# Performance work log

Measured on AMD Instinct MI355X. Metric: run time of the kernel, lower is better.

## Reference

```python
import jax, jax.numpy as jnp
import numpy as np

TOP_K = 2  # config.num_active_experts


def setup_inputs() -> dict:
    key = jax.random.key(0)
    k1, k2, k3, k4 = jax.random.split(key, 4)
    B, S, D = 2, 2048, 1024
    E, W = 8, 1024  # 8 experts, each width 1024 -> total_expert_width = 8192
    x = jax.random.normal(k1, (B, S, D), dtype=jnp.float32)
    router_w = jax.random.normal(k2, (E, D), dtype=jnp.float32) * 0.02
    w1 = jax.random.normal(k3, (D, E * W), dtype=jnp.float32) * 0.02
    w2 = jax.random.normal(k4, (E * W, D), dtype=jnp.float32) * 0.02
    return {"x": x, "router_w": router_w, "w1": w1, "w2": w2}


def reference(x, router_w, w1, w2):
    B, S, D = x.shape
    E = router_w.shape[0]
    W = w1.shape[1] // E  # uniform expert width
    T = B * S
    xf = x.reshape(T, D)

    # Router: sigmoid gating, top-k, sum-normalized weights (norm_topk_prob)
    router_logits = jnp.einsum('td,ed->te', xf, router_w)
    router_probs = jax.nn.sigmoid(router_logits.astype(jnp.float32))
    top_w, sel = jax.lax.top_k(router_probs, TOP_K)          # [T,K]
    top_w = top_w / (top_w.sum(axis=-1, keepdims=True) + 1e-20)
    top_w = top_w.astype(x.dtype)

    # Expert MLPs: expert e uses w1[:, off_e:off_e+W], w2[off_e:off_e+W, :].
    # Uniform width -> single batched einsum over experts (same math as the
    # padded-gather / block-sparse SDD/DSD grouped GEMM pipeline).
    W1e = w1.reshape(D, E, W).transpose(1, 0, 2)             # [E,D,W]
    W2e = w2.reshape(E, W, D)                                # [E,W,D]
    h = jnp.einsum('td,edw->etw', xf, W1e)                   # up-proj
    a = jnp.square(jax.nn.relu(h))                           # relu_squared
    y = jnp.einsum('etw,ewd->etd', a, W2e)                   # down-proj

    # Weighted scatter-combine: combine_weights[t,e] = top_w if e selected else 0
    cw = jnp.zeros((T, E), dtype=x.dtype).at[jnp.arange(T)[:, None], sel].set(top_w)
    out = jnp.einsum('etd,te->td', y, cw)
    return out.reshape(B, S, D)
```

## Files before the change

### kernel.cpp

```cpp
#include <hip/hip_runtime.h>
#include <hip/hip_bf16.h>


#define T_TOKENS 4096
#define DD 1024
#define EE 8
#define WW 1024
#define CAP 1536
#define BM 128
#define BN 64
#define BK 64
#define MT (CAP / BM)
#define NT 16

typedef short bf16x8 __attribute__((ext_vector_type(8)));
typedef float f32x4 __attribute__((ext_vector_type(4)));

__device__ __forceinline__ void gload_lds16(const void* g, void* l) {
  __builtin_amdgcn_global_load_lds((__attribute__((address_space(1))) void*)(g),
                                   (__attribute__((address_space(3))) void*)(l),
                                   16, 0, 0);
}

__device__ __forceinline__ float bf2f(unsigned short u) {
  union { unsigned int i; float f; } v; v.i = (unsigned int)u << 16; return v.f;
}

#define TR_BLOCKS 4096
__global__ __launch_bounds__(256) void pre_kernel(
    const float* __restrict__ w1, const float* __restrict__ w2,
    const float* __restrict__ x, const float* __restrict__ rw,
    __hip_bfloat16* __restrict__ w1t, __hip_bfloat16* __restrict__ w2t,
    __hip_bfloat16* __restrict__ xb, int* __restrict__ sel,
    float* __restrict__ wpair)
{
  __shared__ float tile[64][65];
  int b = blockIdx.x;
  if (b < TR_BLOCKS) {
    int bx = b & 15;
    int by = b >> 4;
    const float* src; __hip_bfloat16* dst;
    long src_ld, dst_ld, c0, r0;
    if (by < 128) {
      src = w1; dst = w1t; src_ld = EE * WW; dst_ld = DD;
      c0 = (long)bx * 64;
      r0 = (long)by * 64;
    } else {
      int z = by - 128;
      int e = z >> 4;
      int yy = z & 15;
      src = w2 + (long)e * WW * DD;
      dst = w2t + (long)e * DD * WW;
      src_ld = DD; dst_ld = WW;
      c0 = (long)bx * 64;
      r0 = (long)yy * 64;
    }
    int tx = threadIdx.x & 15, ty = threadIdx.x >> 4;
#pragma unroll
    for (int i = 0; i < 4; i++) {
      int sr = ty + 16 * i;
      f32x4 v = *(const f32x4*)(src + (c0 + sr) * src_ld + r0 + tx * 4);
      tile[sr][tx * 4 + 0] = v[0];
      tile[sr][tx * 4 + 1] = v[1];
      tile[sr][tx * 4 + 2] = v[2];
      tile[sr][tx * 4 + 3] = v[3];
    }
    __syncthreads();
#pragma unroll
    for (int i = 0; i < 4; i++) {
      int dr = ty + 16 * i;
      union { __hip_bfloat16 hb[4]; ushort4 u4; } pk;
#pragma unroll
      for (int j = 0; j < 4; j++)
        pk.hb[j] = __float2bfloat16(tile[tx * 4 + j][dr]);
      *(ushort4*)((unsigned short*)dst + (r0 + dr) * dst_ld + c0 + tx * 4) = pk.u4;
    }
  } else {
    int lane = threadIdx.x & 63;
    int wave = threadIdx.x >> 6;
    int t = (b - TR_BLOCKS) * 4 + wave;
    const float* xrow = x + (size_t)t * DD;
    float acc[EE];
#pragma unroll
    for (int e = 0; e < EE; e++) acc[e] = 0.f;
#pragma unroll
    for (int i = 0; i < DD / 64; i++) {
      int d = lane + i * 64;
      float xv = xrow[d];
      xb[t * DD + d] = __float2bfloat16(xv);
#pragma unroll
      for (int e = 0; e < EE; e++) acc[e] += xv * rw[e * DD + d];
    }
#pragma unroll
    for (int e = 0; e < EE; e++) {
#pragma unroll
      for (int off = 32; off > 0; off >>= 1)
        acc[e] += __shfl_down(acc[e], off, 64);
    }
    if (lane == 0) {
      float p[EE];
#pragma unroll
      for (int e = 0; e < EE; e++) p[e] = 1.f / (1.f + expf(-acc[e]));
      int e0 = 0; float b0 = p[0];
      for (int e = 1; e < EE; e++) if (p[e] > b0) { b0 = p[e]; e0 = e; }
      int e1 = -1; float b1 = -1.f;
      for (int e = 0; e < EE; e++) {
        if (e == e0) continue;
        if (p[e] > b1) { b1 = p[e]; e1 = e; }
      }
      float s = b0 + b1 + 1e-20f;
      sel[t] = e0 | (e1 << 8);
      wpair[2 * t]     = b0 / s;
      wpair[2 * t + 1] = b1 / s;
    }
  }
}

__global__ __launch_bounds__(1024) void build_lists(
    const int* __restrict__ sel, int* __restrict__ counts,
    int* __restrict__ idx, int* __restrict__ tslot)
{
  __shared__ int lcnt[EE];
  int tid = threadIdx.x, lane = tid & 63;
  if (tid < EE) lcnt[tid] = 0;
  __syncthreads();
  unsigned long long lower = (1ull << lane) - 1;
#pragma unroll
  for (int j = 0; j < T_TOKENS / 1024; j++) {
    int t = j * 1024 + tid;
    int s = sel[t];
    int e0 = s & 0xff, e1 = (s >> 8) & 0xff;
    int slot0 = 0, slot1 = 0;
#pragma unroll
    for (int e = 0; e < EE; e++) {
      unsigned long long m0 = __ballot(e0 == e);
      unsigned long long m1 = __ballot(e1 == e);
      int c0 = __popcll(m0), c1 = __popcll(m1);
      int base = 0;
      if (lane == 0 && (c0 + c1) > 0) base = atomicAdd(&lcnt[e], c0 + c1);
      base = __shfl(base, 0, 64);
      if (e0 == e) slot0 = base + __popcll(m0 & lower);
      if (e1 == e) slot1 = base + c0 + __popcll(m1 & lower);
    }
    int p0 = e0 * CAP + slot0, p1 = e1 * CAP + slot1;
    idx[p0] = t; idx[p1] = t;
    tslot[2 * t] = p0; tslot[2 * t + 1] = p1;
  }
  __syncthreads();
  if (tid < EE) counts[tid] = lcnt[tid];
}

__global__ __launch_bounds__(256) void gemm1_kernel(
    const __hip_bfloat16* __restrict__ xb, const __hip_bfloat16* __restrict__ w1t,
    const int* __restrict__ counts, const int* __restrict__ idx,
    __hip_bfloat16* __restrict__ act)
{
  __shared__ short As[BM * BK];
  __shared__ short Bs[BN * BK];
  int bid = blockIdx.x;
  int e = bid & 7;
  int i = bid >> 3;
  int mt = i >> 4, nt = i & 15;
  int n_e = counts[e];
  if (mt * BM >= n_e) return;

  int tid = threadIdx.x;
  int lane = tid & 63;
  int wave = __builtin_amdgcn_readfirstlane(tid >> 6);
  int wm = (wave >> 1) * 64, wn = (wave & 1) * 32;
  int m16 = lane & 15, qd = lane >> 4;

  const __hip_bfloat16* gA[4];
  const __hip_bfloat16* gB[2];
#pragma unroll
  for (int i2 = 0; i2 < 4; i2++) {
    int s = i2 * 256 + tid;
    int r = s >> 3;
    int q = (s & 7) ^ (r & 7);
    int rowA = mt * BM + r;
    int slot = rowA < n_e ? rowA : n_e - 1;
    int tok = idx[e * CAP + slot];
    gA[i2] = xb + (size_t)tok * DD + q * 8;
  }
#pragma unroll
  for (int i2 = 0; i2 < 2; i2++) {
    int s = i2 * 256 + tid;
    int r = s >> 3;
    int q = (s & 7) ^ (r & 7);
    gB[i2] = w1t + ((size_t)e * WW + nt * BN + r) * DD + q * 8;
  }
  short* ldsA[4];
  short* ldsB[2];
#pragma unroll
  for (int i2 = 0; i2 < 4; i2++) ldsA[i2] = As + (i2 * 256 + wave * 64) * 8;
#pragma unroll
  for (int i2 = 0; i2 < 2; i2++) ldsB[i2] = Bs + (i2 * 256 + wave * 64) * 8;

  int aoff[4][2], boff[2][2];
#pragma unroll
  for (int i2 = 0; i2 < 4; i2++) {
    int r = wm + i2 * 16 + m16;
#pragma unroll
    for (int h = 0; h < 2; h++)
      aoff[i2][h] = (r * 8 + ((qd + h * 4) ^ (r & 7))) * 8;
  }
#pragma unroll
  for (int j = 0; j < 2; j++) {
    int r = wn + j * 16 + m16;
#pragma unroll
    for (int h = 0; h < 2; h++)
      boff[j][h] = (r * 8 + ((qd + h * 4) ^ (r & 7))) * 8;
  }

  f32x4 zero = {0.f, 0.f, 0.f, 0.f};
  f32x4 acc[4][2];
#pragma unroll
  for (int mi = 0; mi < 4; mi++)
#pragma unroll
    for (int ni = 0; ni < 2; ni++) acc[mi][ni] = zero;

  for (int k0 = 0; k0 < DD; k0 += BK) {
    gload_lds16(gA[0] + k0, ldsA[0]);
    gload_lds16(gA[1] + k0, ldsA[1]);
    gload_lds16(gA[2] + k0, ldsA[2]);
    gload_lds16(gA[3] + k0, ldsA[3]);
    gload_lds16(gB[0] + k0, ldsB[0]);
    gload_lds16(gB[1] + k0, ldsB[1]);
    __syncthreads();
#pragma unroll
    for (int h = 0; h < 2; h++) {
      bf16x8 af[4], bfr[2];
#pragma unroll
      for (int i2 = 0; i2 < 4; i2++) af[i2] = *(const bf16x8*)(As + aoff[i2][h]);
#pragma unroll
      for (int j = 0; j < 2; j++) bfr[j] = *(const bf16x8*)(Bs + boff[j][h]);
#pragma unroll
      for (int mi = 0; mi < 4; mi++)
#pragma unroll
        for (int ni = 0; ni < 2; ni++)
          acc[mi][ni] = __builtin_amdgcn_mfma_f32_16x16x32_bf16(
              af[mi], bfr[ni], acc[mi][ni], 0, 0, 0);
    }
    __syncthreads();
  }

#pragma unroll
  for (int mi = 0; mi < 4; mi++) {
#pragma unroll
    for (int reg = 0; reg < 4; reg++) {
      int rowt = mt * BM + wm + mi * 16 + qd * 4 + reg;
      if (rowt < n_e) {
#pragma unroll
        for (int ni = 0; ni < 2; ni++) {
          float v = acc[mi][ni][reg];
          v = v > 0.f ? v * v : 0.f;
          int col = nt * BN + wn + ni * 16 + m16;
          act[((size_t)e * CAP + rowt) * WW + col] = __float2bfloat16(v);
        }
      }
    }
  }
}

__global__ __launch_bounds__(256) void gemm2_kernel(
    const __hip_bfloat16* __restrict__ act, const __hip_bfloat16* __restrict__ w2t,
    const int* __restrict__ counts, __hip_bfloat16* __restrict__ y)
{
  __shared__ short As[BM * BK];
  __shared__ short Bs[BN * BK];
  int bid = blockIdx.x;
  int e = bid & 7;
  int i = bid >> 3;
  int mt = i >> 4, nt = i & 15;
  int n_e = counts[e];
  if (mt * BM >= n_e) return;

  int tid = threadIdx.x;
  int lane = tid & 63;
  int wave = __builtin_amdgcn_readfirstlane(tid >> 6);
  int wm = (wave >> 1) * 64, wn = (wave & 1) * 32;
  int m16 = lane & 15, qd = lane >> 4;

  const __hip_bfloat16* gA[4];
  const __hip_bfloat16* gB[2];
#pragma unroll
  for (int i2 = 0; i2 < 4; i2++) {
    int s = i2 * 256 + tid;
    int r = s >> 3;
    int q = (s & 7) ^ (r & 7);
    gA[i2] = act + ((size_t)e * CAP + mt * BM + r) * WW + q * 8;
  }
#pragma unroll
  for (int i2 = 0; i2 < 2; i2++) {
    int s = i2 * 256 + tid;
    int r = s >> 3;
    int q = (s & 7) ^ (r & 7);
    gB[i2] = w2t + ((size_t)e * DD + nt * BN + r) * WW + q * 8;
  }
  short* ldsA[4];
  short* ldsB[2];
#pragma unroll
  for (int i2 = 0; i2 < 4; i2++) ldsA[i2] = As + (i2 * 256 + wave * 64) * 8;
#pragma unroll
  for (int i2 = 0; i2 < 2; i2++) ldsB[i2] = Bs + (i2 * 256 + wave * 64) * 8;

  int aoff[4][2], boff[2][2];
#pragma unroll
  for (int i2 = 0; i2 < 4; i2++) {
    int r = wm + i2 * 16 + m16;
#pragma unroll
    for (int h = 0; h < 2; h++)
      aoff[i2][h] = (r * 8 + ((qd + h * 4) ^ (r & 7))) * 8;
  }
#pragma unroll
  for (int j = 0; j < 2; j++) {
    int r = wn + j * 16 + m16;
#pragma unroll
    for (int h = 0; h < 2; h++)
      boff[j][h] = (r * 8 + ((qd + h * 4) ^ (r & 7))) * 8;
  }

  f32x4 zero = {0.f, 0.f, 0.f, 0.f};
  f32x4 acc[4][2];
#pragma unroll
  for (int mi = 0; mi < 4; mi++)
#pragma unroll
    for (int ni = 0; ni < 2; ni++) acc[mi][ni] = zero;

  for (int k0 = 0; k0 < WW; k0 += BK) {
    gload_lds16(gA[0] + k0, ldsA[0]);
    gload_lds16(gA[1] + k0, ldsA[1]);
    gload_lds16(gA[2] + k0, ldsA[2]);
    gload_lds16(gA[3] + k0, ldsA[3]);
    gload_lds16(gB[0] + k0, ldsB[0]);
    gload_lds16(gB[1] + k0, ldsB[1]);
    __syncthreads();
#pragma unroll
    for (int h = 0; h < 2; h++) {
      bf16x8 af[4], bfr[2];
#pragma unroll
      for (int i2 = 0; i2 < 4; i2++) af[i2] = *(const bf16x8*)(As + aoff[i2][h]);
#pragma unroll
      for (int j = 0; j < 2; j++) bfr[j] = *(const bf16x8*)(Bs + boff[j][h]);
#pragma unroll
      for (int mi = 0; mi < 4; mi++)
#pragma unroll
        for (int ni = 0; ni < 2; ni++)
          acc[mi][ni] = __builtin_amdgcn_mfma_f32_16x16x32_bf16(
              af[mi], bfr[ni], acc[mi][ni], 0, 0, 0);
    }
    __syncthreads();
  }

#pragma unroll
  for (int mi = 0; mi < 4; mi++) {
#pragma unroll
    for (int reg = 0; reg < 4; reg++) {
      int slot = mt * BM + wm + mi * 16 + qd * 4 + reg;
      if (slot < n_e) {
#pragma unroll
        for (int ni = 0; ni < 2; ni++) {
          int col = nt * BN + wn + ni * 16 + m16;
          y[((size_t)e * CAP + slot) * DD + col] = __float2bfloat16(acc[mi][ni][reg]);
        }
      }
    }
  }
}

__global__ __launch_bounds__(256) void combine_kernel(
    const __hip_bfloat16* __restrict__ y, const int* __restrict__ tslot,
    const float* __restrict__ wpair, float* __restrict__ out)
{
  int t = blockIdx.x;
  int c = threadIdx.x * 4;
  int s0 = tslot[2 * t], s1 = tslot[2 * t + 1];
  float w0 = wpair[2 * t], w1 = wpair[2 * t + 1];
  const unsigned short* yu = (const unsigned short*)y;
  ushort4 a = *(const ushort4*)(yu + (size_t)s0 * DD + c);
  ushort4 bq = *(const ushort4*)(yu + (size_t)s1 * DD + c);
  f32x4 o;
  o[0] = w0 * bf2f(a.x) + w1 * bf2f(bq.x);
  o[1] = w0 * bf2f(a.y) + w1 * bf2f(bq.y);
  o[2] = w0 * bf2f(a.z) + w1 * bf2f(bq.z);
  o[3] = w0 * bf2f(a.w) + w1 * bf2f(bq.w);
  *(f32x4*)(out + (size_t)t * DD + c) = o;
}

extern "C" void kernel_launch(void* const* d_in, const int* in_sizes, int n_in,
                              void* d_out, int out_size, void* d_ws, size_t ws_size,
                              hipStream_t stream)
{
  const float* x  = (const float*)d_in[0];
  const float* rw = (const float*)d_in[1];
  const float* w1 = (const float*)d_in[2];
  const float* w2 = (const float*)d_in[3];
  float* out = (float*)d_out;

  char* ws = (char*)d_ws;
  __hip_bfloat16* xb  = (__hip_bfloat16*)ws;  ws += (size_t)T_TOKENS * DD * 2;
  __hip_bfloat16* w1t = (__hip_bfloat16*)ws;  ws += (size_t)EE * WW * DD * 2;
  __hip_bfloat16* w2t = (__hip_bfloat16*)ws;  ws += (size_t)EE * DD * WW * 2;
  __hip_bfloat16* act = (__hip_bfloat16*)ws;  ws += (size_t)EE * CAP * WW * 2;
  __hip_bfloat16* y   = (__hip_bfloat16*)ws;  ws += (size_t)EE * CAP * DD * 2;
  int*   counts = (int*)ws;                   ws += 256;
  int*   idx    = (int*)ws;                   ws += (size_t)EE * CAP * 4;
  int*   sel    = (int*)ws;                   ws += (size_t)T_TOKENS * 4;
  int*   tslot  = (int*)ws;                   ws += (size_t)T_TOKENS * 8;
  float* wpair  = (float*)ws;                 ws += (size_t)T_TOKENS * 8;

  pre_kernel<<<TR_BLOCKS + T_TOKENS / 4, 256, 0, stream>>>(
      w1, w2, x, rw, w1t, w2t, xb, sel, wpair);
  build_lists<<<1, 1024, 0, stream>>>(sel, counts, idx, tslot);
  gemm1_kernel<<<EE * MT * NT, 256, 0, stream>>>(xb, w1t, counts, idx, act);
  gemm2_kernel<<<EE * MT * NT, 256, 0, stream>>>(act, w2t, counts, y);
  combine_kernel<<<T_TOKENS, 256, 0, stream>>>(y, tslot, wpair, out);
}
```

Before: 193.7 us.

## Fuse weight fp32-to-bf16 conversion into GEMM B-tile staging, drop transpose pass

Removes the separate pre-pass that transposed and converted w1/w2 into bf16 workspace copies. Each GEMM now loads fp32 weight columns directly, converts them to bf16 in registers, and writes them swizzled into LDS. This saves a full read and write of 64 MB of weights plus the transpose kernel. In exchange the B loads move from async global-to-LDS to synchronous register loads, the fp32 data is re-read by every M-tile block, and each thread's loads are strided rows of 64 floats.

Measured after the change: 204.9 us. 5.8% more time.

```diff
diff --git a/kernel.cpp b/kernel.cpp
--- a/kernel.cpp
+++ b/kernel.cpp
@@ -26,93 +26,47 @@
   union { unsigned int i; float f; } v; v.i = (unsigned int)u << 16; return v.f;
 }
 
-#define TR_BLOCKS 4096
-__global__ __launch_bounds__(256) void pre_kernel(
-    const float* __restrict__ w1, const float* __restrict__ w2,
+__global__ __launch_bounds__(256) void router_kernel(
     const float* __restrict__ x, const float* __restrict__ rw,
-    __hip_bfloat16* __restrict__ w1t, __hip_bfloat16* __restrict__ w2t,
     __hip_bfloat16* __restrict__ xb, int* __restrict__ sel,
     float* __restrict__ wpair)
 {
-  __shared__ float tile[64][65];
-  int b = blockIdx.x;
-  if (b < TR_BLOCKS) {
-    int bx = b & 15;
-    int by = b >> 4;
-    const float* src; __hip_bfloat16* dst;
-    long src_ld, dst_ld, c0, r0;
-    if (by < 128) {
-      src = w1; dst = w1t; src_ld = EE * WW; dst_ld = DD;
-      c0 = (long)bx * 64;
-      r0 = (long)by * 64;
-    } else {
-      int z = by - 128;
-      int e = z >> 4;
-      int yy = z & 15;
-      src = w2 + (long)e * WW * DD;
-      dst = w2t + (long)e * DD * WW;
-      src_ld = DD; dst_ld = WW;
-      c0 = (long)bx * 64;
-      r0 = (long)yy * 64;
-    }
-    int tx = threadIdx.x & 15, ty = threadIdx.x >> 4;
-#pragma unroll
-    for (int i = 0; i < 4; i++) {
-      int sr = ty + 16 * i;
-      f32x4 v = *(const f32x4*)(src + (c0 + sr) * src_ld + r0 + tx * 4);
-      tile[sr][tx * 4 + 0] = v[0];
-      tile[sr][tx * 4 + 1] = v[1];
-      tile[sr][tx * 4 + 2] = v[2];
-      tile[sr][tx * 4 + 3] = v[3];
-    }
-    __syncthreads();
-#pragma unroll
-    for (int i = 0; i < 4; i++) {
-      int dr = ty + 16 * i;
-      union { __hip_bfloat16 hb[4]; ushort4 u4; } pk;
-#pragma unroll
-      for (int j = 0; j < 4; j++)
-        pk.hb[j] = __float2bfloat16(tile[tx * 4 + j][dr]);
-      *(ushort4*)((unsigned short*)dst + (r0 + dr) * dst_ld + c0 + tx * 4) = pk.u4;
-    }
-  } else {
-    int lane = threadIdx.x & 63;
-    int wave = threadIdx.x >> 6;
-    int t = (b - TR_BLOCKS) * 4 + wave;
-    const float* xrow = x + (size_t)t * DD;
-    float acc[EE];
-#pragma unroll
-    for (int e = 0; e < EE; e++) acc[e] = 0.f;
-#pragma unroll
-    for (int i = 0; i < DD / 64; i++) {
-      int d = lane + i * 64;
-      float xv = xrow[d];
-      xb[t * DD + d] = __float2bfloat16(xv);
-#pragma unroll
-      for (int e = 0; e < EE; e++) acc[e] += xv * rw[e * DD + d];
-    }
-#pragma unroll
+  int lane = threadIdx.x & 63;
+  int wave = threadIdx.x >> 6;
+  int t = blockIdx.x * 4 + wave;
+  const float* xrow = x + (size_t)t * DD;
+  float acc[EE];
+#pragma unroll
+  for (int e = 0; e < EE; e++) acc[e] = 0.f;
+#pragma unroll
+  for (int i = 0; i < DD / 64; i++) {
+    int d = lane + i * 64;
+    float xv = xrow[d];
+    xb[t * DD + d] = __float2bfloat16(xv);
+#pragma unroll
+    for (int e = 0; e < EE; e++) acc[e] += xv * rw[e * DD + d];
+  }
+#pragma unroll
+  for (int e = 0; e < EE; e++) {
+#pragma unroll
+    for (int off = 32; off > 0; off >>= 1)
+      acc[e] += __shfl_down(acc[e], off, 64);
+  }
+  if (lane == 0) {
+    float p[EE];
+#pragma unroll
+    for (int e = 0; e < EE; e++) p[e] = 1.f / (1.f + expf(-acc[e]));
+    int e0 = 0; float b0 = p[0];
+    for (int e = 1; e < EE; e++) if (p[e] > b0) { b0 = p[e]; e0 = e; }
+    int e1 = -1; float b1 = -1.f;
     for (int e = 0; e < EE; e++) {
-#pragma unroll
-      for (int off = 32; off > 0; off >>= 1)
-        acc[e] += __shfl_down(acc[e], off, 64);
-    }
-    if (lane == 0) {
-      float p[EE];
-#pragma unroll
-      for (int e = 0; e < EE; e++) p[e] = 1.f / (1.f + expf(-acc[e]));
-      int e0 = 0; float b0 = p[0];
-      for (int e = 1; e < EE; e++) if (p[e] > b0) { b0 = p[e]; e0 = e; }
-      int e1 = -1; float b1 = -1.f;
-      for (int e = 0; e < EE; e++) {
-        if (e == e0) continue;
-        if (p[e] > b1) { b1 = p[e]; e1 = e; }
-      }
-      float s = b0 + b1 + 1e-20f;
-      sel[t] = e0 | (e1 << 8);
-      wpair[2 * t]     = b0 / s;
-      wpair[2 * t + 1] = b1 / s;
-    }
+      if (e == e0) continue;
+      if (p[e] > b1) { b1 = p[e]; e1 = e; }
+    }
+    float s = b0 + b1 + 1e-20f;
+    sel[t] = e0 | (e1 << 8);
+    wpair[2 * t]     = b0 / s;
+    wpair[2 * t + 1] = b1 / s;
   }
 }
 
@@ -150,8 +104,26 @@
   if (tid < EE) counts[tid] = lcnt[tid];
 }
 
+__device__ __forceinline__ void stage_B_cvt(
+    const float* __restrict__ bp, size_t ldb, short* __restrict__ Bs,
+    int n_loc, int kq)
+{
+  float v[16];
+#pragma unroll
+  for (int j = 0; j < 16; j++) v[j] = bp[(size_t)j * ldb];
+  union { short s[8]; bf16x8 vec; } lo, hi;
+#pragma unroll
+  for (int j = 0; j < 8; j++) {
+    lo.s[j] = (short)__bfloat16_as_ushort(__float2bfloat16(v[j]));
+    hi.s[j] = (short)__bfloat16_as_ushort(__float2bfloat16(v[j + 8]));
+  }
+  int sw = n_loc & 7;
+  *(bf16x8*)(Bs + (n_loc * 8 + ((2 * kq) ^ sw)) * 8) = lo.vec;
+  *(bf16x8*)(Bs + (n_loc * 8 + ((2 * kq + 1) ^ sw)) * 8) = hi.vec;
+}
+
 __global__ __launch_bounds__(256) void gemm1_kernel(
-    const __hip_bfloat16* __restrict__ xb, const __hip_bfloat16* __restrict__ w1t,
+    const __hip_bfloat16* __restrict__ xb, const float* __restrict__ w1,
     const int* __restrict__ counts, const int* __restrict__ idx,
     __hip_bfloat16* __restrict__ act)
 {
@@ -171,7 +143,6 @@
   int m16 = lane & 15, qd = lane >> 4;
 
   const __hip_bfloat16* gA[4];
-  const __hip_bfloat16* gB[2];
 #pragma unroll
   for (int i2 = 0; i2 < 4; i2++) {
     int s = i2 * 256 + tid;
@@ -182,19 +153,14 @@
     int tok = idx[e * CAP + slot];
     gA[i2] = xb + (size_t)tok * DD + q * 8;
   }
-#pragma unroll
-  for (int i2 = 0; i2 < 2; i2++) {
-    int s = i2 * 256 + tid;
-    int r = s >> 3;
-    int q = (s & 7) ^ (r & 7);
-    gB[i2] = w1t + ((size_t)e * WW + nt * BN + r) * DD + q * 8;
-  }
   short* ldsA[4];
-  short* ldsB[2];
 #pragma unroll
   for (int i2 = 0; i2 < 4; i2++) ldsA[i2] = As + (i2 * 256 + wave * 64) * 8;
-#pragma unroll
-  for (int i2 = 0; i2 < 2; i2++) ldsB[i2] = Bs + (i2 * 256 + wave * 64) * 8;
+
+  int n_loc = tid & 63;
+  int kq = tid >> 6;
+  const float* bp = w1 + (size_t)(kq * 16) * (EE * WW)
+                       + (size_t)e * WW + nt * BN + n_loc;
 
   int aoff[4][2], boff[2][2];
 #pragma unroll
@@ -224,8 +190,8 @@
     gload_lds16(gA[1] + k0, ldsA[1]);
     gload_lds16(gA[2] + k0, ldsA[2]);
     gload_lds16(gA[3] + k0, ldsA[3]);
-    gload_lds16(gB[0] + k0, ldsB[0]);
-    gload_lds16(gB[1] + k0, ldsB[1]);
+    stage_B_cvt(bp, EE * WW, Bs, n_loc, kq);
+    bp += (size_t)BK * (EE * WW);
     __syncthreads();
 #pragma unroll
     for (int h = 0; h < 2; h++) {
@@ -263,7 +229,7 @@
 }
 
 __global__ __launch_bounds__(256) void gemm2_kernel(
-    const __hip_bfloat16* __restrict__ act, const __hip_bfloat16* __restrict__ w2t,
+    const __hip_bfloat16* __restrict__ act, const float* __restrict__ w2,
     const int* __restrict__ counts, __hip_bfloat16* __restrict__ y)
 {
   __shared__ short As[BM * BK];
@@ -282,7 +248,6 @@
   int m16 = lane & 15, qd = lane >> 4;
 
   const __hip_bfloat16* gA[4];
-  const __hip_bfloat16* gB[2];
 #pragma unroll
   for (int i2 = 0; i2 < 4; i2++) {
     int s = i2 * 256 + tid;
@@ -290,19 +255,13 @@
     int q = (s & 7) ^ (r & 7);
     gA[i2] = act + ((size_t)e * CAP + mt * BM + r) * WW + q * 8;
   }
-#pragma unroll
-  for (int i2 = 0; i2 < 2; i2++) {
-    int s = i2 * 256 + tid;
-    int r = s >> 3;
-    int q = (s & 7) ^ (r & 7);
-    gB[i2] = w2t + ((size_t)e * DD + nt * BN + r) * WW + q * 8;
-  }
   short* ldsA[4];
-  short* ldsB[2];
 #pragma unroll
   for (int i2 = 0; i2 < 4; i2++) ldsA[i2] = As + (i2 * 256 + wave * 64) * 8;
-#pragma unroll
-  for (int i2 = 0; i2 < 2; i2++) ldsB[i2] = Bs + (i2 * 256 + wave * 64) * 8;
+
+  int n_loc = tid & 63;
+  int kq = tid >> 6;
+  const float* bp = w2 + ((size_t)e * WW + kq * 16) * DD + nt * BN + n_loc;
 
   int aoff[4][2], boff[2][2];
 #pragma unroll
@@ -332,8 +291,8 @@
     gload_lds16(gA[1] + k0, ldsA[1]);
     gload_lds16(gA[2] + k0, ldsA[2]);
     gload_lds16(gA[3] + k0, ldsA[3]);
-    gload_lds16(gB[0] + k0, ldsB[0]);
-    gload_lds16(gB[1] + k0, ldsB[1]);
+    stage_B_cvt(bp, DD, Bs, n_loc, kq);
+    bp += (size_t)BK * DD;
     __syncthreads();
 #pragma unroll
     for (int h = 0; h < 2; h++) {
@@ -399,8 +358,6 @@
 
   char* ws = (char*)d_ws;
   __hip_bfloat16* xb  = (__hip_bfloat16*)ws;  ws += (size_t)T_TOKENS * DD * 2;
-  __hip_bfloat16* w1t = (__hip_bfloat16*)ws;  ws += (size_t)EE * WW * DD * 2;
-  __hip_bfloat16* w2t = (__hip_bfloat16*)ws;  ws += (size_t)EE * DD * WW * 2;
   __hip_bfloat16* act = (__hip_bfloat16*)ws;  ws += (size_t)EE * CAP * WW * 2;
   __hip_bfloat16* y   = (__hip_bfloat16*)ws;  ws += (size_t)EE * CAP * DD * 2;
   int*   counts = (int*)ws;                   ws += 256;
@@ -409,10 +366,9 @@
   int*   tslot  = (int*)ws;                   ws += (size_t)T_TOKENS * 8;
   float* wpair  = (float*)ws;                 ws += (size_t)T_TOKENS * 8;
 
-  pre_kernel<<<TR_BLOCKS + T_TOKENS / 4, 256, 0, stream>>>(
-      w1, w2, x, rw, w1t, w2t, xb, sel, wpair);
+  router_kernel<<<T_TOKENS / 4, 256, 0, stream>>>(x, rw, xb, sel, wpair);
   build_lists<<<1, 1024, 0, stream>>>(sel, counts, idx, tslot);
-  gemm1_kernel<<<EE * MT * NT, 256, 0, stream>>>(xb, w1t, counts, idx, act);
-  gemm2_kernel<<<EE * MT * NT, 256, 0, stream>>>(act, w2t, counts, y);
+  gemm1_kernel<<<EE * MT * NT, 256, 0, stream>>>(xb, w1, counts, idx, act);
+  gemm2_kernel<<<EE * MT * NT, 256, 0, stream>>>(act, w2, counts, y);
   combine_kernel<<<T_TOKENS, 256, 0, stream>>>(y, tslot, wpair, out);
 }
```

## Double-buffer LDS tiles in both expert GEMM kernels to overlap loads with MFMA

Applied to the files above, without the earlier changes.

Both grouped GEMM kernels now keep two LDS buffers for the A and B tiles. Before the loop a prologue loads the first k-tile. Each iteration then issues global-to-LDS loads for the next k-tile into the alternate buffer before running MFMAs on the current one, with one barrier per iteration instead of two. The goal is to hide global load latency behind matrix compute. In exchange, LDS use per block doubles to about 48 KB, which can reduce how many blocks fit on each CU.

Measured after the change: 216.6 us. 1.12x slower.

```diff
diff --git a/kernel.cpp b/kernel.cpp
--- a/kernel.cpp
+++ b/kernel.cpp
@@ -12,6 +12,8 @@
 #define BK 64
 #define MT (CAP / BM)
 #define NT 16
+#define ABUF (BM * BK)
+#define BBUF (BN * BK)
 
 typedef short bf16x8 __attribute__((ext_vector_type(8)));
 typedef float f32x4 __attribute__((ext_vector_type(4)));
@@ -155,8 +157,8 @@
     const int* __restrict__ counts, const int* __restrict__ idx,
     __hip_bfloat16* __restrict__ act)
 {
-  __shared__ short As[BM * BK];
-  __shared__ short Bs[BN * BK];
+  __shared__ short As[2 * ABUF];
+  __shared__ short Bs[2 * BBUF];
   int bid = blockIdx.x;
   int e = bid & 7;
   int i = bid >> 3;
@@ -189,12 +191,12 @@
     int q = (s & 7) ^ (r & 7);
     gB[i2] = w1t + ((size_t)e * WW + nt * BN + r) * DD + q * 8;
   }
-  short* ldsA[4];
-  short* ldsB[2];
-#pragma unroll
-  for (int i2 = 0; i2 < 4; i2++) ldsA[i2] = As + (i2 * 256 + wave * 64) * 8;
-#pragma unroll
-  for (int i2 = 0; i2 < 2; i2++) ldsB[i2] = Bs + (i2 * 256 + wave * 64) * 8;
+  short* stA[4];
+  short* stB[2];
+#pragma unroll
+  for (int i2 = 0; i2 < 4; i2++) stA[i2] = As + (i2 * 256 + wave * 64) * 8;
+#pragma unroll
+  for (int i2 = 0; i2 < 2; i2++) stB[i2] = Bs + (i2 * 256 + wave * 64) * 8;
 
   int aoff[4][2], boff[2][2];
 #pragma unroll
@@ -219,21 +221,32 @@
 #pragma unroll
     for (int ni = 0; ni < 2; ni++) acc[mi][ni] = zero;
 
+#pragma unroll
+  for (int i2 = 0; i2 < 4; i2++) gload_lds16(gA[i2], stA[i2]);
+#pragma unroll
+  for (int i2 = 0; i2 < 2; i2++) gload_lds16(gB[i2], stB[i2]);
+  __syncthreads();
+
+  int p = 0;
   for (int k0 = 0; k0 < DD; k0 += BK) {
-    gload_lds16(gA[0] + k0, ldsA[0]);
-    gload_lds16(gA[1] + k0, ldsA[1]);
-    gload_lds16(gA[2] + k0, ldsA[2]);
-    gload_lds16(gA[3] + k0, ldsA[3]);
-    gload_lds16(gB[0] + k0, ldsB[0]);
-    gload_lds16(gB[1] + k0, ldsB[1]);
-    __syncthreads();
+    int np = p ^ 1;
+    if (k0 + BK < DD) {
+      gload_lds16(gA[0] + k0 + BK, stA[0] + np * ABUF);
+      gload_lds16(gA[1] + k0 + BK, stA[1] + np * ABUF);
+      gload_lds16(gA[2] + k0 + BK, stA[2] + np * ABUF);
+      gload_lds16(gA[3] + k0 + BK, stA[3] + np * ABUF);
+      gload_lds16(gB[0] + k0 + BK, stB[0] + np * BBUF);
+      gload_lds16(gB[1] + k0 + BK, stB[1] + np * BBUF);
+    }
+    const short* Ab = As + p * ABUF;
+    const short* Bb = Bs + p * BBUF;
 #pragma unroll
     for (int h = 0; h < 2; h++) {
       bf16x8 af[4], bfr[2];
 #pragma unroll
-      for (int i2 = 0; i2 < 4; i2++) af[i2] = *(const bf16x8*)(As + aoff[i2][h]);
-#pragma unroll
-      for (int j = 0; j < 2; j++) bfr[j] = *(const bf16x8*)(Bs + boff[j][h]);
+      for (int i2 = 0; i2 < 4; i2++) af[i2] = *(const bf16x8*)(Ab + aoff[i2][h]);
+#pragma unroll
+      for (int j = 0; j < 2; j++) bfr[j] = *(const bf16x8*)(Bb + boff[j][h]);
 #pragma unroll
       for (int mi = 0; mi < 4; mi++)
 #pragma unroll
@@ -242,6 +255,7 @@
               af[mi], bfr[ni], acc[mi][ni], 0, 0, 0);
     }
     __syncthreads();
+    p = np;
   }
 
 #pragma unroll
@@ -266,8 +280,8 @@
     const __hip_bfloat16* __restrict__ act, const __hip_bfloat16* __restrict__ w2t,
     const int* __restrict__ counts, __hip_bfloat16* __restrict__ y)
 {
-  __shared__ short As[BM * BK];
-  __shared__ short Bs[BN * BK];
+  __shared__ short As[2 * ABUF];
+  __shared__ short Bs[2 * BBUF];
   int bid = blockIdx.x;
   int e = bid & 7;
   int i = bid >> 3;
@@ -297,12 +311,12 @@
     int q = (s & 7) ^ (r & 7);
     gB[i2] = w2t + ((size_t)e * DD + nt * BN + r) * WW + q * 8;
   }
-  short* ldsA[4];
-  short* ldsB[2];
-#pragma unroll
-  for (int i2 = 0; i2 < 4; i2++) ldsA[i2] = As + (i2 * 256 + wave * 64) * 8;
-#pragma unroll
-  for (int i2 = 0; i2 < 2; i2++) ldsB[i2] = Bs + (i2 * 256 + wave * 64) * 8;
+  short* stA[4];
+  short* stB[2];
+#pragma unroll
+  for (int i2 = 0; i2 < 4; i2++) stA[i2] = As + (i2 * 256 + wave * 64) * 8;
+#pragma unroll
+  for (int i2 = 0; i2 < 2; i2++) stB[i2] = Bs + (i2 * 256 + wave * 64) * 8;
 
   int aoff[4][2], boff[2][2];
 #pragma unroll
@@ -327,21 +341,32 @@
 #pragma unroll
     for (int ni = 0; ni < 2; ni++) acc[mi][ni] = zero;
 
+#pragma unroll
+  for (int i2 = 0; i2 < 4; i2++) gload_lds16(gA[i2], stA[i2]);
+#pragma unroll
+  for (int i2 = 0; i2 < 2; i2++) gload_lds16(gB[i2], stB[i2]);
+  __syncthreads();
+
+  int p = 0;
   for (int k0 = 0; k0 < WW; k0 += BK) {
-    gload_lds16(gA[0] + k0, ldsA[0]);
-    gload_lds16(gA[1] + k0, ldsA[1]);
-    gload_lds16(gA[2] + k0, ldsA[2]);
-    gload_lds16(gA[3] + k0, ldsA[3]);
-    gload_lds16(gB[0] + k0, ldsB[0]);
-    gload_lds16(gB[1] + k0, ldsB[1]);
-    __syncthreads();
+    int np = p ^ 1;
+    if (k0 + BK < WW) {
+      gload_lds16(gA[0] + k0 + BK, stA[0] + np * ABUF);
+      gload_lds16(gA[1] + k0 + BK, stA[1] + np * ABUF);
+      gload_lds16(gA[2] + k0 + BK, stA[2] + np * ABUF);
+      gload_lds16(gA[3] + k0 + BK, stA[3] + np * ABUF);
+      gload_lds16(gB[0] + k0 + BK, stB[0] + np * BBUF);
+      gload_lds16(gB[1] + k0 + BK, stB[1] + np * BBUF);
+    }
+    const short* Ab = As + p * ABUF;
+    const short* Bb = Bs + p * BBUF;
 #pragma unroll
     for (int h = 0; h < 2; h++) {
       bf16x8 af[4], bfr[2];
 #pragma unroll
-      for (int i2 = 0; i2 < 4; i2++) af[i2] = *(const bf16x8*)(As + aoff[i2][h]);
-#pragma unroll
-      for (int j = 0; j < 2; j++) bfr[j] = *(const bf16x8*)(Bs + boff[j][h]);
+      for (int i2 = 0; i2 < 4; i2++) af[i2] = *(const bf16x8*)(Ab + aoff[i2][h]);
+#pragma unroll
+      for (int j = 0; j < 2; j++) bfr[j] = *(const bf16x8*)(Bb + boff[j][h]);
 #pragma unroll
       for (int mi = 0; mi < 4; mi++)
 #pragma unroll
@@ -350,6 +375,7 @@
               af[mi], bfr[ni], acc[mi][ni], 0, 0, 0);
     }
     __syncthreads();
+    p = np;
   }
 
 #pragma unroll
```

## Move w2 transpose-convert into gemm1 launch to overlap with expert GEMM

Applied to the files above, without the earlier changes.

The w2 fp32-to-bf16 transpose is taken out of the pre kernel and appended as extra blocks in the gemm1 launch, sharing its LDS buffer. The pre kernel then only handles w1, x and the router, and the w2 conversion runs alongside the first expert GEMM instead of before build_lists. This is meant to hide bandwidth-bound transpose work behind the gemm1 tail and shorten the serial critical path. The cost is a larger gemm1 grid, with transpose blocks competing with GEMM blocks for CUs and memory bandwidth.

Result: no change. 194.8 us (+0.5%).

```diff
diff --git a/kernel.cpp b/kernel.cpp
--- a/kernel.cpp
+++ b/kernel.cpp
@@ -12,6 +12,8 @@
 #define BK 64
 #define MT (CAP / BM)
 #define NT 16
+#define G1_BLOCKS (EE * MT * NT)
+#define W2T_BLOCKS 2048
 
 typedef short bf16x8 __attribute__((ext_vector_type(8)));
 typedef float f32x4 __attribute__((ext_vector_type(4)));
@@ -26,40 +28,25 @@
   union { unsigned int i; float f; } v; v.i = (unsigned int)u << 16; return v.f;
 }
 
-#define TR_BLOCKS 4096
+#define TR1_BLOCKS 2048
 __global__ __launch_bounds__(256) void pre_kernel(
-    const float* __restrict__ w1, const float* __restrict__ w2,
-    const float* __restrict__ x, const float* __restrict__ rw,
-    __hip_bfloat16* __restrict__ w1t, __hip_bfloat16* __restrict__ w2t,
+    const float* __restrict__ w1, const float* __restrict__ x,
+    const float* __restrict__ rw, __hip_bfloat16* __restrict__ w1t,
     __hip_bfloat16* __restrict__ xb, int* __restrict__ sel,
     float* __restrict__ wpair)
 {
   __shared__ float tile[64][65];
   int b = blockIdx.x;
-  if (b < TR_BLOCKS) {
+  if (b < TR1_BLOCKS) {
     int bx = b & 15;
     int by = b >> 4;
-    const float* src; __hip_bfloat16* dst;
-    long src_ld, dst_ld, c0, r0;
-    if (by < 128) {
-      src = w1; dst = w1t; src_ld = EE * WW; dst_ld = DD;
-      c0 = (long)bx * 64;
-      r0 = (long)by * 64;
-    } else {
-      int z = by - 128;
-      int e = z >> 4;
-      int yy = z & 15;
-      src = w2 + (long)e * WW * DD;
-      dst = w2t + (long)e * DD * WW;
-      src_ld = DD; dst_ld = WW;
-      c0 = (long)bx * 64;
-      r0 = (long)yy * 64;
-    }
+    long c0 = (long)bx * 64;
+    long r0 = (long)by * 64;
     int tx = threadIdx.x & 15, ty = threadIdx.x >> 4;
 #pragma unroll
     for (int i = 0; i < 4; i++) {
       int sr = ty + 16 * i;
-      f32x4 v = *(const f32x4*)(src + (c0 + sr) * src_ld + r0 + tx * 4);
+      f32x4 v = *(const f32x4*)(w1 + (c0 + sr) * (EE * WW) + r0 + tx * 4);
       tile[sr][tx * 4 + 0] = v[0];
       tile[sr][tx * 4 + 1] = v[1];
       tile[sr][tx * 4 + 2] = v[2];
@@ -73,12 +60,12 @@
 #pragma unroll
       for (int j = 0; j < 4; j++)
         pk.hb[j] = __float2bfloat16(tile[tx * 4 + j][dr]);
-      *(ushort4*)((unsigned short*)dst + (r0 + dr) * dst_ld + c0 + tx * 4) = pk.u4;
+      *(ushort4*)((unsigned short*)w1t + (r0 + dr) * DD + c0 + tx * 4) = pk.u4;
     }
   } else {
     int lane = threadIdx.x & 63;
     int wave = threadIdx.x >> 6;
-    int t = (b - TR_BLOCKS) * 4 + wave;
+    int t = (b - TR1_BLOCKS) * 4 + wave;
     const float* xrow = x + (size_t)t * DD;
     float acc[EE];
 #pragma unroll
@@ -150,10 +137,157 @@
   if (tid < EE) counts[tid] = lcnt[tid];
 }
 
-__global__ __launch_bounds__(256) void gemm1_kernel(
+__global__ __launch_bounds__(256) void gemm1_fused(
     const __hip_bfloat16* __restrict__ xb, const __hip_bfloat16* __restrict__ w1t,
     const int* __restrict__ counts, const int* __restrict__ idx,
-    __hip_bfloat16* __restrict__ act)
+    __hip_bfloat16* __restrict__ act,
+    const float* __restrict__ w2, __hip_bfloat16* __restrict__ w2t)
+{
+  __shared__ short smem[BM * BK + BN * BK];
+  int bid = blockIdx.x;
+  int tid = threadIdx.x;
+
+  if (bid >= G1_BLOCKS) {
+    int tb = bid - G1_BLOCKS;
+    int bx = tb & 15;
+    int z = tb >> 4;
+    int e = z >> 4, yy = z & 15;
+    const float* src = w2 + (long)e * WW * DD;
+    __hip_bfloat16* dst = w2t + (long)e * DD * WW;
+    long c0 = (long)bx * 64;
+    long r0 = (long)yy * 64;
+    float (*tile)[65] = (float(*)[65])smem;
+    int tx = tid & 15, ty = tid >> 4;
+#pragma unroll
+    for (int i = 0; i < 4; i++) {
+      int sr = ty + 16 * i;
+      f32x4 v = *(const f32x4*)(src + (c0 + sr) * DD + r0 + tx * 4);
+      tile[sr][tx * 4 + 0] = v[0];
+      tile[sr][tx * 4 + 1] = v[1];
+      tile[sr][tx * 4 + 2] = v[2];
+      tile[sr][tx * 4 + 3] = v[3];
+    }
+    __syncthreads();
+#pragma unroll
+    for (int i = 0; i < 4; i++) {
+      int dr = ty + 16 * i;
+      union { __hip_bfloat16 hb[4]; ushort4 u4; } pk;
+#pragma unroll
+      for (int j = 0; j < 4; j++)
+        pk.hb[j] = __float2bfloat16(tile[tx * 4 + j][dr]);
+      *(ushort4*)((unsigned short*)dst + (r0 + dr) * WW + c0 + tx * 4) = pk.u4;
+    }
+    return;
+  }
+
+  short* As = smem;
+  short* Bs = smem + BM * BK;
+  int e = bid & 7;
+  int i = bid >> 3;
+  int mt = i >> 4, nt = i & 15;
+  int n_e = counts[e];
+  if (mt * BM >= n_e) return;
+
+  int lane = tid & 63;
+  int wave = __builtin_amdgcn_readfirstlane(tid >> 6);
+  int wm = (wave >> 1) * 64, wn = (wave & 1) * 32;
+  int m16 = lane & 15, qd = lane >> 4;
+
+  const __hip_bfloat16* gA[4];
+  const __hip_bfloat16* gB[2];
+#pragma unroll
+  for (int i2 = 0; i2 < 4; i2++) {
+    int s = i2 * 256 + tid;
+    int r = s >> 3;
+    int q = (s & 7) ^ (r & 7);
+    int rowA = mt * BM + r;
+    int slot = rowA < n_e ? rowA : n_e - 1;
+    int tok = idx[e * CAP + slot];
+    gA[i2] = xb + (size_t)tok * DD + q * 8;
+  }
+#pragma unroll
+  for (int i2 = 0; i2 < 2; i2++) {
+    int s = i2 * 256 + tid;
+    int r = s >> 3;
+    int q = (s & 7) ^ (r & 7);
+    gB[i2] = w1t + ((size_t)e * WW + nt * BN + r) * DD + q * 8;
+  }
+  short* stA[4];
+  short* stB[2];
+#pragma unroll
+  for (int i2 = 0; i2 < 4; i2++) stA[i2] = As + (i2 * 256 + wave * 64) * 8;
+#pragma unroll
+  for (int i2 = 0; i2 < 2; i2++) stB[i2] = Bs + (i2 * 256 + wave * 64) * 8;
+
+  int aoff[4][2], boff[2][2];
+#pragma unroll
+  for (int i2 = 0; i2 < 4; i2++) {
+    int r = wm + i2 * 16 + m16;
+#pragma unroll
+    for (int h = 0; h < 2; h++)
+      aoff[i2][h] = (r * 8 + ((qd + h * 4) ^ (r & 7))) * 8;
+  }
+#pragma unroll
+  for (int j = 0; j < 2; j++) {
+    int r = wn + j * 16 + m16;
+#pragma unroll
+    for (int h = 0; h < 2; h++)
+      boff[j][h] = (r * 8 + ((qd + h * 4) ^ (r & 7))) * 8;
+  }
+
+  f32x4 zero = {0.f, 0.f, 0.f, 0.f};
+  f32x4 acc[4][2];
+#pragma unroll
+  for (int mi = 0; mi < 4; mi++)
+#pragma unroll
+    for (int ni = 0; ni < 2; ni++) acc[mi][ni] = zero;
+
+  for (int k0 = 0; k0 < DD; k0 += BK) {
+    gload_lds16(gA[0] + k0, stA[0]);
+    gload_lds16(gA[1] + k0, stA[1]);
+    gload_lds16(gA[2] + k0, stA[2]);
+    gload_lds16(gA[3] + k0, stA[3]);
+    gload_lds16(gB[0] + k0, stB[0]);
+    gload_lds16(gB[1] + k0, stB[1]);
+    __syncthreads();
+#pragma unroll
+    for (int h = 0; h < 2; h++) {
+      bf16x8 af[4], bfr[2];
+#pragma unroll
+      for (int i2 = 0; i2 < 4; i2++) af[i2] = *(const bf16x8*)(As + aoff[i2][h]);
+#pragma unroll
+      for (int j = 0; j < 2; j++) bfr[j] = *(const bf16x8*)(Bs + boff[j][h]);
+#pragma unroll
+      for (int mi = 0; mi < 4; mi++)
+#pragma unroll
+        for (int ni = 0; ni < 2; ni++)
+          acc[mi][ni] = __builtin_amdgcn_mfma_f32_16x16x32_bf16(
+              af[mi], bfr[ni], acc[mi][ni], 0, 0, 0);
+    }
+    __syncthreads();
+  }
+
+#pragma unroll
+  for (int mi = 0; mi < 4; mi++) {
+#pragma unroll
+    for (int reg = 0; reg < 4; reg++) {
+      int rowt = mt * BM + wm + mi * 16 + qd * 4 + reg;
+      if (rowt < n_e) {
+#pragma unroll
+        for (int ni = 0; ni < 2; ni++) {
+          float v = acc[mi][ni][reg];
+          v = v > 0.f ? v * v : 0.f;
+          int col = nt * BN + wn + ni * 16 + m16;
+          act[((size_t)e * CAP + rowt) * WW + col] = __float2bfloat16(v);
+        }
+      }
+    }
+  }
+}
+
+__global__ __launch_bounds__(256) void gemm2_kernel(
+    const __hip_bfloat16* __restrict__ act, const __hip_bfloat16* __restrict__ w2t,
+    const int* __restrict__ counts, __hip_bfloat16* __restrict__ y)
 {
   __shared__ short As[BM * BK];
   __shared__ short Bs[BN * BK];
@@ -177,117 +311,6 @@
     int s = i2 * 256 + tid;
     int r = s >> 3;
     int q = (s & 7) ^ (r & 7);
-    int rowA = mt * BM + r;
-    int slot = rowA < n_e ? rowA : n_e - 1;
-    int tok = idx[e * CAP + slot];
-    gA[i2] = xb + (size_t)tok * DD + q * 8;
-  }
-#pragma unroll
-  for (int i2 = 0; i2 < 2; i2++) {
-    int s = i2 * 256 + tid;
-    int r = s >> 3;
-    int q = (s & 7) ^ (r & 7);
-    gB[i2] = w1t + ((size_t)e * WW + nt * BN + r) * DD + q * 8;
-  }
-  short* ldsA[4];
-  short* ldsB[2];
-#pragma unroll
-  for (int i2 = 0; i2 < 4; i2++) ldsA[i2] = As + (i2 * 256 + wave * 64) * 8;
-#pragma unroll
-  for (int i2 = 0; i2 < 2; i2++) ldsB[i2] = Bs + (i2 * 256 + wave * 64) * 8;
-
-  int aoff[4][2], boff[2][2];
-#pragma unroll
-  for (int i2 = 0; i2 < 4; i2++) {
-    int r = wm + i2 * 16 + m16;
-#pragma unroll
-    for (int h = 0; h < 2; h++)
-      aoff[i2][h] = (r * 8 + ((qd + h * 4) ^ (r & 7))) * 8;
-  }
-#pragma unroll
-  for (int j = 0; j < 2; j++) {
-    int r = wn + j * 16 + m16;
-#pragma unroll
-    for (int h = 0; h < 2; h++)
-      boff[j][h] = (r * 8 + ((qd + h * 4) ^ (r & 7))) * 8;
-  }
-
-  f32x4 zero = {0.f, 0.f, 0.f, 0.f};
-  f32x4 acc[4][2];
-#pragma unroll
-  for (int mi = 0; mi < 4; mi++)
-#pragma unroll
-    for (int ni = 0; ni < 2; ni++) acc[mi][ni] = zero;
-
-  for (int k0 = 0; k0 < DD; k0 += BK) {
-    gload_lds16(gA[0] + k0, ldsA[0]);
-    gload_lds16(gA[1] + k0, ldsA[1]);
-    gload_lds16(gA[2] + k0, ldsA[2]);
-    gload_lds16(gA[3] + k0, ldsA[3]);
-    gload_lds16(gB[0] + k0, ldsB[0]);
-    gload_lds16(gB[1] + k0, ldsB[1]);
-    __syncthreads();
-#pragma unroll
-    for (int h = 0; h < 2; h++) {
-      bf16x8 af[4], bfr[2];
-#pragma unroll
-      for (int i2 = 0; i2 < 4; i2++) af[i2] = *(const bf16x8*)(As + aoff[i2][h]);
-#pragma unroll
-      for (int j = 0; j < 2; j++) bfr[j] = *(const bf16x8*)(Bs + boff[j][h]);
-#pragma unroll
-      for (int mi = 0; mi < 4; mi++)
-#pragma unroll
-        for (int ni = 0; ni < 2; ni++)
-          acc[mi][ni] = __builtin_amdgcn_mfma_f32_16x16x32_bf16(
-              af[mi], bfr[ni], acc[mi][ni], 0, 0, 0);
-    }
-    __syncthreads();
-  }
-
-#pragma unroll
-  for (int mi = 0; mi < 4; mi++) {
-#pragma unroll
-    for (int reg = 0; reg < 4; reg++) {
-      int rowt = mt * BM + wm + mi * 16 + qd * 4 + reg;
-      if (rowt < n_e) {
-#pragma unroll
-        for (int ni = 0; ni < 2; ni++) {
-          float v = acc[mi][ni][reg];
-          v = v > 0.f ? v * v : 0.f;
-          int col = nt * BN + wn + ni * 16 + m16;
-          act[((size_t)e * CAP + rowt) * WW + col] = __float2bfloat16(v);
-        }
-      }
-    }
-  }
-}
-
-__global__ __launch_bounds__(256) void gemm2_kernel(
-    const __hip_bfloat16* __restrict__ act, const __hip_bfloat16* __restrict__ w2t,
-    const int* __restrict__ counts, __hip_bfloat16* __restrict__ y)
-{
-  __shared__ short As[BM * BK];
-  __shared__ short Bs[BN * BK];
-  int bid = blockIdx.x;
-  int e = bid & 7;
-  int i = bid >> 3;
-  int mt = i >> 4, nt = i & 15;
-  int n_e = counts[e];
-  if (mt * BM >= n_e) return;
-
-  int tid = threadIdx.x;
-  int lane = tid & 63;
-  int wave = __builtin_amdgcn_readfirstlane(tid >> 6);
-  int wm = (wave >> 1) * 64, wn = (wave & 1) * 32;
-  int m16 = lane & 15, qd = lane >> 4;
-
-  const __hip_bfloat16* gA[4];
-  const __hip_bfloat16* gB[2];
-#pragma unroll
-  for (int i2 = 0; i2 < 4; i2++) {
-    int s = i2 * 256 + tid;
-    int r = s >> 3;
-    int q = (s & 7) ^ (r & 7);
     gA[i2] = act + ((size_t)e * CAP + mt * BM + r) * WW + q * 8;
   }
 #pragma unroll
@@ -297,12 +320,12 @@
     int q = (s & 7) ^ (r & 7);
     gB[i2] = w2t + ((size_t)e * DD + nt * BN + r) * WW + q * 8;
   }
-  short* ldsA[4];
-  short* ldsB[2];
-#pragma unroll
-  for (int i2 = 0; i2 < 4; i2++) ldsA[i2] = As + (i2 * 256 + wave * 64) * 8;
-#pragma unroll
-  for (int i2 = 0; i2 < 2; i2++) ldsB[i2] = Bs + (i2 * 256 + wave * 64) * 8;
+  short* stA[4];
+  short* stB[2];
+#pragma unroll
+  for (int i2 = 0; i2 < 4; i2++) stA[i2] = As + (i2 * 256 + wave * 64) * 8;
+#pragma unroll
+  for (int i2 = 0; i2 < 2; i2++) stB[i2] = Bs + (i2 * 256 + wave * 64) * 8;
 
   int aoff[4][2], boff[2][2];
 #pragma unroll
@@ -328,12 +351,12 @@
     for (int ni = 0; ni < 2; ni++) acc[mi][ni] = zero;
 
   for (int k0 = 0; k0 < WW; k0 += BK) {
-    gload_lds16(gA[0] + k0, ldsA[0]);
-    gload_lds16(gA[1] + k0, ldsA[1]);
-    gload_lds16(gA[2] + k0, ldsA[2]);
-    gload_lds16(gA[3] + k0, ldsA[3]);
-    gload_lds16(gB[0] + k0, ldsB[0]);
-    gload_lds16(gB[1] + k0, ldsB[1]);
+    gload_lds16(gA[0] + k0, stA[0]);
+    gload_lds16(gA[1] + k0, stA[1]);
+    gload_lds16(gA[2] + k0, stA[2]);
+    gload_lds16(gA[3] + k0, stA[3]);
+    gload_lds16(gB[0] + k0, stB[0]);
+    gload_lds16(gB[1] + k0, stB[1]);
     __syncthreads();
 #pragma unroll
     for (int h = 0; h < 2; h++) {
@@ -409,10 +432,11 @@
   int*   tslot  = (int*)ws;                   ws += (size_t)T_TOKENS * 8;
   float* wpair  = (float*)ws;                 ws += (size_t)T_TOKENS * 8;
 
-  pre_kernel<<<TR_BLOCKS + T_TOKENS / 4, 256, 0, stream>>>(
-      w1, w2, x, rw, w1t, w2t, xb, sel, wpair);
+  pre_kernel<<<TR1_BLOCKS + T_TOKENS / 4, 256, 0, stream>>>(
+      w1, x, rw, w1t, xb, sel, wpair);
   build_lists<<<1, 1024, 0, stream>>>(sel, counts, idx, tslot);
-  gemm1_kernel<<<EE * MT * NT, 256, 0, stream>>>(xb, w1t, counts, idx, act);
+  gemm1_fused<<<G1_BLOCKS + W2T_BLOCKS, 256, 0, stream>>>(
+      xb, w1t, counts, idx, act, w2, w2t);
   gemm2_kernel<<<EE * MT * NT, 256, 0, stream>>>(act, w2t, counts, y);
   combine_kernel<<<T_TOKENS, 256, 0, stream>>>(y, tslot, wpair, out);
 }
```
